# Kernel tuning notes

Measured on AMD Instinct MI355X. Metric: run time of the kernel, lower is better.

Reference implementation:

```python
import jax, jax.numpy as jnp
import numpy as np


def setup_inputs() -> dict:
    key = jax.random.key(0)
    k1, k2 = jax.random.split(key)
    z = jax.random.normal(k1, (16, 256, 32, 32), dtype=jnp.float32)
    emb = jax.random.normal(k2, (8192, 256), dtype=jnp.float32)
    return {"z": z, "emb": emb}


def reference(z, emb):
    B, C, H, W = z.shape
    # [B,C,H,W] -> [B*H*W, C], distances in fp32 for precision
    z_f = jnp.transpose(z, (0, 2, 3, 1)).reshape(-1, C).astype(jnp.float32)
    e = emb.astype(jnp.float32)
    # squared-distance expansion: ||z||^2 - 2 z.e + ||e||^2  -> [N, K]
    d = (
        jnp.sum(z_f * z_f, axis=1, keepdims=True)
        - 2.0 * (z_f @ e.T)
        + jnp.sum(e * e, axis=1)[None, :]
    )
    idx = jnp.argmin(d, axis=1)  # [N]
    out = emb[idx].astype(z.dtype)  # codebook gather
    return jnp.transpose(out.reshape(B, H, W, C), (0, 3, 1, 2))
```

## Files before the change

kernel.cpp:

```cpp
#include <hip/hip_runtime.h>
#include <stdint.h>

#define NB   16
#define CD   256
#define HW   1024
#define NQ   16384
#define KCN  8192

typedef unsigned long long u64;
typedef unsigned short     u16;
using f32x4  = __attribute__((ext_vector_type(4))) float;
using bf16x8 = __attribute__((ext_vector_type(8))) __bf16;

#define ZTB_OFF  0
#define EMBB_OFF 8388608
#define EH_OFF   12582912
#define CAND_OFF 12615680

static __device__ __forceinline__ void gl_lds16(const void* g, void* l) {
  __builtin_amdgcn_global_load_lds(
      (const __attribute__((address_space(1))) void*)g,
      (__attribute__((address_space(3))) void*)l, 16, 0, 0);
}

static __device__ __forceinline__ unsigned bf16r(float x) {
  unsigned u = __float_as_uint(x);
  return (u + 0x7fffu + ((u >> 16) & 1u)) >> 16;
}

static __device__ __forceinline__ u64 umin64(u64 a, u64 b) { return a < b ? a : b; }
static __device__ __forceinline__ u64 umax64(u64 a, u64 b) { return a < b ? b : a; }

__global__ __launch_bounds__(256) void k_prep(const float* __restrict__ z,
                                              const float* __restrict__ emb,
                                              u16* __restrict__ zTb,
                                              u16* __restrict__ embB,
                                              float* __restrict__ eH) {
  const int bx = (int)blockIdx.x;
  if (bx < 1024) {
    __shared__ float tile[64][65];
    const int b   = bx >> 6;
    const int hwT = (bx >> 2) & 15;
    const int cT  = bx & 3;
    const int tx  = threadIdx.x & 63;
    const int ty  = threadIdx.x >> 6;
    const float* src = z + (size_t)(b * CD + cT * 64) * HW + hwT * 64;
#pragma unroll
    for (int i = 0; i < 16; ++i) {
      const int c_l = ty + 4 * i;
      tile[c_l][tx] = src[(size_t)c_l * HW + tx];
    }
    __syncthreads();
    const size_t dbase = (size_t)(b * HW + hwT * 64) * CD + cT * 64;
#pragma unroll
    for (int i = 0; i < 16; ++i) {
      const int hw_l = ty + 4 * i;
      zTb[dbase + (size_t)hw_l * CD + tx] = (u16)bf16r(tile[tx][hw_l]);
    }
  } else {
    const int wave = (bx - 1024) * 4 + ((int)threadIdx.x >> 6);
    const int lane = threadIdx.x & 63;
#pragma unroll
    for (int it = 0; it < 8; ++it) {
      const int row = wave * 8 + it;
      const float4 v = *(const float4*)(emb + (size_t)row * CD + lane * 4);
      uint2 pk;
      pk.x = bf16r(v.x) | (bf16r(v.y) << 16);
      pk.y = bf16r(v.z) | (bf16r(v.w) << 16);
      *(uint2*)(embB + (size_t)row * CD + lane * 4) = pk;
      float s = v.x * v.x + v.y * v.y + v.z * v.z + v.w * v.w;
#pragma unroll
      for (int off = 32; off; off >>= 1) s += __shfl_xor(s, off, 64);
      if (lane == 0) eH[row] = 0.5f * s + 1024.0f;
    }
  }
}

#define NT  8
#define BKC 4

__global__ __launch_bounds__(256, 2) void k_argmin(const u16* __restrict__ zTb,
                                                   const u16* __restrict__ embB,
                                                   const float* __restrict__ eH,
                                                   u64* __restrict__ cand) {
  __shared__ __align__(16) u16 As[128 * 64];
  __shared__ __align__(16) u16 Bs[128 * 64];
  const int tid  = threadIdx.x;
  const int w    = tid >> 6;
  const int lane = tid & 63;
  const int l15  = lane & 15, quad = lane >> 4, l7 = lane & 7;
  const int q0    = (int)(blockIdx.x >> 3) * 128;
  const int split = (int)(blockIdx.x & 7);
  const int wq0 = (w & 1) * 64, wn0 = (w >> 1) * 64, wh = w >> 1;

  const int srow  = w * 32 + (lane >> 3);
  const int scol8 = (l7 ^ (lane >> 3)) * 8;
  const int ldsL  = w * 4096 + lane * 16;
  const int co0 = ((0 * 4 + quad) ^ l7) * 16;
  const int co1 = ((1 * 4 + quad) ^ l7) * 16;

  const float FMAX = __uint_as_float(0x7F7FFFFFu);
  float b1[16], b2[16];
#pragma unroll
  for (int s = 0; s < 16; ++s) { b1[s] = FMAX; b2[s] = FMAX; }

  for (int nt = 0; nt < NT; ++nt) {
    const int n0 = split * 1024 + nt * 128;
    float eh[4];
#pragma unroll
    for (int j = 0; j < 4; ++j) eh[j] = eH[n0 + wn0 + 16 * j + l15];

    f32x4 acc[4][4];
#pragma unroll
    for (int i = 0; i < 4; ++i)
#pragma unroll
      for (int j = 0; j < 4; ++j) acc[i][j] = f32x4{0.f, 0.f, 0.f, 0.f};

    for (int kc = 0; kc < BKC; ++kc) {
#pragma unroll
      for (int i = 0; i < 4; ++i) {
        const int row = srow + i * 8;
        gl_lds16(zTb  + (size_t)(q0 + row) * CD + kc * 64 + scol8,
                 (char*)As + ldsL + i * 1024);
        gl_lds16(embB + (size_t)(n0 + row) * CD + kc * 64 + scol8,
                 (char*)Bs + ldsL + i * 1024);
      }
      __syncthreads();
#pragma unroll
      for (int ks = 0; ks < 2; ++ks) {
        const int co = ks ? co1 : co0;
        bf16x8 af[4], bfr[4];
#pragma unroll
        for (int i = 0; i < 4; ++i)
          af[i] = *(const bf16x8*)((const char*)As + (wq0 + i * 16 + l15) * 128 + co);
#pragma unroll
        for (int j = 0; j < 4; ++j)
          bfr[j] = *(const bf16x8*)((const char*)Bs + (wn0 + j * 16 + l15) * 128 + co);
#pragma unroll
        for (int i = 0; i < 4; ++i)
#pragma unroll
          for (int j = 0; j < 4; ++j)
            acc[i][j] = __builtin_amdgcn_mfma_f32_16x16x32_bf16(af[i], bfr[j],
                                                                acc[i][j], 0, 0, 0);
      }
      __syncthreads();
    }
#pragma unroll
    for (int i = 0; i < 4; ++i) {
#pragma unroll
      for (int r = 0; r < 4; ++r) {
        const int s = i * 4 + r;
        float kq[4];
#pragma unroll
        for (int j = 0; j < 4; ++j) {
          const unsigned kb = (__float_as_uint(eh[j] - acc[i][j][r]) & ~31u)
                              | (unsigned)(nt * 4 + j);
          kq[j] = __uint_as_float(kb);
        }
        const float lo01 = fminf(kq[0], kq[1]), hi01 = fmaxf(kq[0], kq[1]);
        const float lo23 = fminf(kq[2], kq[3]), hi23 = fmaxf(kq[2], kq[3]);
        const float best = fminf(lo01, lo23);
        const float sec  = fminf(fmaxf(lo01, lo23), fminf(hi01, hi23));
        b2[s] = fminf(fmaxf(best, b1[s]), fminf(sec, b2[s]));
        b1[s] = fminf(best, b1[s]);
      }
    }
  }
#pragma unroll
  for (int s = 0; s < 16; ++s) {
    u64 x1 = ((u64)__float_as_uint(b1[s]) << 32) | (unsigned)l15;
    u64 x2 = ((u64)__float_as_uint(b2[s]) << 32) | (unsigned)l15;
#pragma unroll
    for (int off = 1; off < 16; off <<= 1) {
      const u64 o1 = __shfl_xor(x1, off, 64);
      const u64 o2 = __shfl_xor(x2, off, 64);
      const u64 lo = umin64(x1, o1);
      const u64 hi = umax64(x1, o1);
      x1 = lo;
      x2 = umin64(hi, umin64(x2, o2));
    }
    if (l15 == 0) {
      const int i = s >> 2, r = s & 3;
      const int q = q0 + wq0 + i * 16 + quad * 4 + r;
      const unsigned kb1 = (unsigned)(x1 >> 32), kb2 = (unsigned)(x2 >> 32);
      const int n1 = split * 1024 + (int)((kb1 >> 2) & 7) * 128 + wn0
                     + 16 * (int)(kb1 & 3) + (int)(x1 & 15);
      const int n2 = split * 1024 + (int)((kb2 >> 2) & 7) * 128 + wn0
                     + 16 * (int)(kb2 & 3) + (int)(x2 & 15);
      cand[(size_t)q * 32 + split * 4 + wh * 2 + 0] = ((u64)kb1 << 32) | (unsigned)n1;
      cand[(size_t)q * 32 + split * 4 + wh * 2 + 1] = ((u64)kb2 << 32) | (unsigned)n2;
    }
  }
}

__global__ __launch_bounds__(256) void k_pick_out(const float* __restrict__ z,
                                                  const float* __restrict__ emb,
                                                  const u64* __restrict__ cand,
                                                  float* __restrict__ out) {
  __shared__ float zs[16][257];
  __shared__ float tile[16][257];
  const int t    = (int)threadIdx.x;
  const int lane = t & 63;
  const int wv   = t >> 6;
  const int sub  = lane >> 4;
  const int l15  = lane & 15;
  const int q0b  = (int)blockIdx.x * 16;
  const int b    = q0b >> 10, hw0 = q0b & 1023;
  const int q    = q0b + wv * 4 + sub;
  const int hwl  = wv * 4 + sub;

  {
    const float* zp = z + ((size_t)(b * CD + t)) * HW + hw0;
    const float4 a0 = *(const float4*)(zp + 0);
    const float4 a1 = *(const float4*)(zp + 4);
    const float4 a2 = *(const float4*)(zp + 8);
    const float4 a3 = *(const float4*)(zp + 12);
    zs[0][t] = a0.x;  zs[1][t] = a0.y;  zs[2][t] = a0.z;  zs[3][t] = a0.w;
    zs[4][t] = a1.x;  zs[5][t] = a1.y;  zs[6][t] = a1.z;  zs[7][t] = a1.w;
    zs[8][t] = a2.x;  zs[9][t] = a2.y;  zs[10][t] = a2.z; zs[11][t] = a2.w;
    zs[12][t] = a3.x; zs[13][t] = a3.y; zs[14][t] = a3.z; zs[15][t] = a3.w;
  }
  __syncthreads();

  const u64* cp = cand + (size_t)q * 32 + l15 * 2;
  const u64 v0 = cp[0], v1 = cp[1];
  u64 s0 = umin64(v0, v1), s1 = umax64(v0, v1), s2 = ~0ull, s3 = ~0ull;
#pragma unroll
  for (int off = 1; off < 16; off <<= 1) {
    const u64 b0 = __shfl_xor(s0, off, 64);
    const u64 b1 = __shfl_xor(s1, off, 64);
    const u64 b2 = __shfl_xor(s2, off, 64);
    const u64 b3 = __shfl_xor(s3, off, 64);
    const u64 c0 = umin64(s0, b0);
    const u64 c1 = umin64(umin64(s1, b1), umax64(s0, b0));
    const u64 c2 = umin64(umin64(s2, b2),
                          umin64(umax64(s1, b0), umax64(s0, b1)));
    const u64 c3 = umin64(umin64(umin64(s3, b3), umax64(s2, b0)),
                          umin64(umax64(s0, b2), umax64(s1, b1)));
    s0 = c0; s1 = c1; s2 = c2; s3 = c3;
  }
  const u64 sel[4] = {s0, s1, s2, s3};

  float zq[16];
#pragma unroll
  for (int j = 0; j < 16; ++j) zq[j] = zs[hwl][j * 16 + l15];

  double bd = 1e300;
  int bi = 0x7fffffff;
  float keep[16];
#pragma unroll
  for (int j = 0; j < 16; ++j) keep[j] = 0.f;
#pragma unroll
  for (int c4 = 0; c4 < 4; ++c4) {
    const int idx = (int)(unsigned)(sel[c4] & 0xffffffffull);
    const float* er = emb + (size_t)idx * CD;
    float ev[16];
#pragma unroll
    for (int j = 0; j < 16; ++j) ev[j] = er[j * 16 + l15];
    double s = 0.0;
#pragma unroll
    for (int j = 0; j < 16; ++j) {
      const double d = (double)zq[j] - (double)ev[j];
      s += d * d;
    }
#pragma unroll
    for (int off = 1; off < 16; off <<= 1) s += __shfl_xor(s, off, 64);
    const bool better = (s < bd) || (s == bd && idx < bi);
    if (better) {
      bd = s; bi = idx;
#pragma unroll
      for (int j = 0; j < 16; ++j) keep[j] = ev[j];
    }
  }
#pragma unroll
  for (int j = 0; j < 16; ++j) tile[hwl][j * 16 + l15] = keep[j];
  __syncthreads();
  const int cluster = t >> 4;
  const int ll      = t & 15;
  float* obase = out + (size_t)b * CD * HW + hw0 + ll;
#pragma unroll
  for (int j = 0; j < 16; ++j) {
    const int c = 16 * j + cluster;
    obase[(size_t)c * HW] = tile[ll][c];
  }
}

extern "C" void kernel_launch(void* const* d_in, const int* in_sizes, int n_in,
                              void* d_out, int out_size, void* d_ws, size_t ws_size,
                              hipStream_t stream) {
  const float* z   = (const float*)d_in[0];
  const float* emb = (const float*)d_in[1];
  float* out = (float*)d_out;

  char* ws = (char*)d_ws;
  u16*   zTb  = (u16*)(ws + ZTB_OFF);
  u16*   embB = (u16*)(ws + EMBB_OFF);
  float* eH   = (float*)(ws + EH_OFF);
  u64*   cand = (u64*)(ws + CAND_OFF);

  k_prep<<<1280, 256, 0, stream>>>(z, emb, zTb, embB, eH);
  k_argmin<<<1024, 256, 0, stream>>>(zTb, embB, eH, cand);
  k_pick_out<<<1024, 256, 0, stream>>>(z, emb, cand, out);
}
```

Baseline: 181.8 us.

## Load query operand directly into registers with double-buffered prefetch, drop A LDS tile

The query (A) tile is no longer staged through shared memory. Each wave loads its MFMA A fragments straight from global memory into registers and prefetches the next k-chunk into a second register buffer while the current one is consumed. Only the codebook (B) tile still goes through LDS. This halves LDS traffic and footprint, but A is reloaded from global/L2 every n-tile (8 times) and register pressure rises, which could hurt the 2-blocks-per-CU occupancy target.

Measured after the change: 214.2 us. 1.18x slower.

```diff
diff --git a/kernel.cpp b/kernel.cpp
--- a/kernel.cpp
+++ b/kernel.cpp
@@ -77,13 +77,11 @@
 }
 
 #define NT  8
-#define BKC 4
 
 __global__ __launch_bounds__(256, 2) void k_argmin(const u16* __restrict__ zTb,
                                                    const u16* __restrict__ embB,
                                                    const float* __restrict__ eH,
                                                    u64* __restrict__ cand) {
-  __shared__ __align__(16) u16 As[128 * 64];
   __shared__ __align__(16) u16 Bs[128 * 64];
   const int tid  = threadIdx.x;
   const int w    = tid >> 6;
@@ -93,16 +91,58 @@
   const int split = (int)(blockIdx.x & 7);
   const int wq0 = (w & 1) * 64, wn0 = (w >> 1) * 64, wh = w >> 1;
 
-  const int srow  = w * 32 + (lane >> 3);
+  const int srowB = w * 32 + (lane >> 3);
   const int scol8 = (l7 ^ (lane >> 3)) * 8;
   const int ldsL  = w * 4096 + lane * 16;
   const int co0 = ((0 * 4 + quad) ^ l7) * 16;
   const int co1 = ((1 * 4 + quad) ^ l7) * 16;
 
+  const u16* abase = zTb + (size_t)(q0 + wq0 + l15) * CD + quad * 8;
+
   const float FMAX = __uint_as_float(0x7F7FFFFFu);
   float b1[16], b2[16];
 #pragma unroll
   for (int s = 0; s < 16; ++s) { b1[s] = FMAX; b2[s] = FMAX; }
+
+  f32x4 acc[4][4];
+
+  bf16x8 aA[8], aB[8];
+#pragma unroll
+  for (int i = 0; i < 4; ++i)
+#pragma unroll
+    for (int ks = 0; ks < 2; ++ks)
+      aA[i * 2 + ks] = *(const bf16x8*)(abase + (size_t)i * 16 * CD + ks * 32);
+
+#define KSTEP(CUR, NXT, KC, KCN)                                                   \
+  do {                                                                             \
+    _Pragma("unroll")                                                              \
+    for (int i = 0; i < 4; ++i)                                                    \
+      gl_lds16(embB + (size_t)(n0 + srowB + i * 8) * CD + (KC) * 64 + scol8,       \
+               (char*)Bs + ldsL + i * 1024);                                       \
+    _Pragma("unroll")                                                              \
+    for (int i = 0; i < 4; ++i)                                                    \
+      _Pragma("unroll")                                                            \
+      for (int ks = 0; ks < 2; ++ks)                                               \
+        NXT[i * 2 + ks] =                                                          \
+            *(const bf16x8*)(abase + (size_t)i * 16 * CD + (KCN) * 64 + ks * 32);  \
+    __syncthreads();                                                               \
+    _Pragma("unroll")                                                              \
+    for (int ks = 0; ks < 2; ++ks) {                                               \
+      const int co = ks ? co1 : co0;                                               \
+      bf16x8 bfr[4];                                                               \
+      _Pragma("unroll")                                                            \
+      for (int j = 0; j < 4; ++j)                                                  \
+        bfr[j] = *(const bf16x8*)((const char*)Bs + (wn0 + j * 16 + l15) * 128 + co); \
+      _Pragma("unroll")                                                            \
+      for (int i = 0; i < 4; ++i)                                                  \
+        _Pragma("unroll")                                                          \
+        for (int j = 0; j < 4; ++j)                                                \
+          acc[i][j] = __builtin_amdgcn_mfma_f32_16x16x32_bf16(CUR[i * 2 + ks],     \
+                                                              bfr[j], acc[i][j],   \
+                                                              0, 0, 0);            \
+    }                                                                              \
+    __syncthreads();                                                               \
+  } while (0)
 
   for (int nt = 0; nt < NT; ++nt) {
     const int n0 = split * 1024 + nt * 128;
@@ -110,41 +150,16 @@
 #pragma unroll
     for (int j = 0; j < 4; ++j) eh[j] = eH[n0 + wn0 + 16 * j + l15];
 
-    f32x4 acc[4][4];
 #pragma unroll
     for (int i = 0; i < 4; ++i)
 #pragma unroll
       for (int j = 0; j < 4; ++j) acc[i][j] = f32x4{0.f, 0.f, 0.f, 0.f};
 
-    for (int kc = 0; kc < BKC; ++kc) {
-#pragma unroll
-      for (int i = 0; i < 4; ++i) {
-        const int row = srow + i * 8;
-        gl_lds16(zTb  + (size_t)(q0 + row) * CD + kc * 64 + scol8,
-                 (char*)As + ldsL + i * 1024);
-        gl_lds16(embB + (size_t)(n0 + row) * CD + kc * 64 + scol8,
-                 (char*)Bs + ldsL + i * 1024);
-      }
-      __syncthreads();
-#pragma unroll
-      for (int ks = 0; ks < 2; ++ks) {
-        const int co = ks ? co1 : co0;
-        bf16x8 af[4], bfr[4];
-#pragma unroll
-        for (int i = 0; i < 4; ++i)
-          af[i] = *(const bf16x8*)((const char*)As + (wq0 + i * 16 + l15) * 128 + co);
-#pragma unroll
-        for (int j = 0; j < 4; ++j)
-          bfr[j] = *(const bf16x8*)((const char*)Bs + (wn0 + j * 16 + l15) * 128 + co);
-#pragma unroll
-        for (int i = 0; i < 4; ++i)
-#pragma unroll
-          for (int j = 0; j < 4; ++j)
-            acc[i][j] = __builtin_amdgcn_mfma_f32_16x16x32_bf16(af[i], bfr[j],
-                                                                acc[i][j], 0, 0, 0);
-      }
-      __syncthreads();
-    }
+    KSTEP(aA, aB, 0, 1);
+    KSTEP(aB, aA, 1, 2);
+    KSTEP(aA, aB, 2, 3);
+    KSTEP(aB, aA, 3, 0);
+
 #pragma unroll
     for (int i = 0; i < 4; ++i) {
 #pragma unroll
@@ -166,6 +181,8 @@
       }
     }
   }
+#undef KSTEP
+
 #pragma unroll
   for (int s = 0; s < 16; ++s) {
     u64 x1 = ((u64)__float_as_uint(b1[s]) << 32) | (unsigned)l15;
```

## Double-buffer LDS tiles to overlap global-to-LDS loads with MFMA compute

Applied to the files above, without the earlier changes.

Adds a second pair of shared-memory A/B tiles and prefetches the next K chunk (including the first chunk of the next N tile) into the idle buffer while MFMAs run on the current one. This removes the serialized load, sync, compute pattern and one barrier per K step. It doubles LDS use to 64KB per block, which may reduce occupancy under launch_bounds(256,2). The final iteration issues a redundant prefetch, and correctness depends on the direct-to-LDS loads having completed by the barrier.

Result: faster. 177.9 us (-2.2%).

```diff
diff --git a/kernel.cpp b/kernel.cpp
--- a/kernel.cpp
+++ b/kernel.cpp
@@ -77,14 +77,15 @@
 }
 
 #define NT  8
-#define BKC 4
 
 __global__ __launch_bounds__(256, 2) void k_argmin(const u16* __restrict__ zTb,
                                                    const u16* __restrict__ embB,
                                                    const float* __restrict__ eH,
                                                    u64* __restrict__ cand) {
-  __shared__ __align__(16) u16 As[128 * 64];
-  __shared__ __align__(16) u16 Bs[128 * 64];
+  __shared__ __align__(16) u16 As0[128 * 64];
+  __shared__ __align__(16) u16 Bs0[128 * 64];
+  __shared__ __align__(16) u16 As1[128 * 64];
+  __shared__ __align__(16) u16 Bs1[128 * 64];
   const int tid  = threadIdx.x;
   const int w    = tid >> 6;
   const int lane = tid & 63;
@@ -104,47 +105,68 @@
 #pragma unroll
   for (int s = 0; s < 16; ++s) { b1[s] = FMAX; b2[s] = FMAX; }
 
+  f32x4 acc[4][4];
+
+  {
+    const int n0i = split * 1024;
+#pragma unroll
+    for (int i = 0; i < 4; ++i) {
+      const int row = srow + i * 8;
+      gl_lds16(zTb  + (size_t)(q0 + row) * CD + 0 * 64 + scol8,
+               (char*)As0 + ldsL + i * 1024);
+      gl_lds16(embB + (size_t)(n0i + row) * CD + 0 * 64 + scol8,
+               (char*)Bs0 + ldsL + i * 1024);
+    }
+  }
+  __syncthreads();
+
+#define KSTEP(PA, PB, NA, NBuf, NKC, NN0)                                            \
+  do {                                                                               \
+    _Pragma("unroll")                                                                \
+    for (int i = 0; i < 4; ++i) {                                                    \
+      const int row = srow + i * 8;                                                  \
+      gl_lds16(zTb  + (size_t)(q0 + row) * CD + (NKC) * 64 + scol8,                  \
+               (char*)NA + ldsL + i * 1024);                                         \
+      gl_lds16(embB + (size_t)((NN0) + row) * CD + (NKC) * 64 + scol8,               \
+               (char*)NBuf + ldsL + i * 1024);                                       \
+    }                                                                                \
+    _Pragma("unroll")                                                                \
+    for (int ks = 0; ks < 2; ++ks) {                                                 \
+      const int co = ks ? co1 : co0;                                                 \
+      bf16x8 af[4], bfr[4];                                                          \
+      _Pragma("unroll")                                                              \
+      for (int i = 0; i < 4; ++i)                                                    \
+        af[i] = *(const bf16x8*)((const char*)PA + (wq0 + i * 16 + l15) * 128 + co); \
+      _Pragma("unroll")                                                              \
+      for (int j = 0; j < 4; ++j)                                                    \
+        bfr[j] = *(const bf16x8*)((const char*)PB + (wn0 + j * 16 + l15) * 128 + co);\
+      _Pragma("unroll")                                                              \
+      for (int i = 0; i < 4; ++i)                                                    \
+        _Pragma("unroll")                                                            \
+        for (int j = 0; j < 4; ++j)                                                  \
+          acc[i][j] = __builtin_amdgcn_mfma_f32_16x16x32_bf16(af[i], bfr[j],         \
+                                                              acc[i][j], 0, 0, 0);   \
+    }                                                                                \
+    __syncthreads();                                                                 \
+  } while (0)
+
   for (int nt = 0; nt < NT; ++nt) {
-    const int n0 = split * 1024 + nt * 128;
+    const int n0  = split * 1024 + nt * 128;
+    const int n0n = (nt == NT - 1) ? n0 : n0 + 128;
     float eh[4];
 #pragma unroll
     for (int j = 0; j < 4; ++j) eh[j] = eH[n0 + wn0 + 16 * j + l15];
 
-    f32x4 acc[4][4];
 #pragma unroll
     for (int i = 0; i < 4; ++i)
 #pragma unroll
       for (int j = 0; j < 4; ++j) acc[i][j] = f32x4{0.f, 0.f, 0.f, 0.f};
 
-    for (int kc = 0; kc < BKC; ++kc) {
-#pragma unroll
-      for (int i = 0; i < 4; ++i) {
-        const int row = srow + i * 8;
-        gl_lds16(zTb  + (size_t)(q0 + row) * CD + kc * 64 + scol8,
-                 (char*)As + ldsL + i * 1024);
-        gl_lds16(embB + (size_t)(n0 + row) * CD + kc * 64 + scol8,
-                 (char*)Bs + ldsL + i * 1024);
-      }
-      __syncthreads();
-#pragma unroll
-      for (int ks = 0; ks < 2; ++ks) {
-        const int co = ks ? co1 : co0;
-        bf16x8 af[4], bfr[4];
-#pragma unroll
-        for (int i = 0; i < 4; ++i)
-          af[i] = *(const bf16x8*)((const char*)As + (wq0 + i * 16 + l15) * 128 + co);
-#pragma unroll
-        for (int j = 0; j < 4; ++j)
-          bfr[j] = *(const bf16x8*)((const char*)Bs + (wn0 + j * 16 + l15) * 128 + co);
-#pragma unroll
-        for (int i = 0; i < 4; ++i)
-#pragma unroll
-          for (int j = 0; j < 4; ++j)
-            acc[i][j] = __builtin_amdgcn_mfma_f32_16x16x32_bf16(af[i], bfr[j],
-                                                                acc[i][j], 0, 0, 0);
-      }
-      __syncthreads();
-    }
+    KSTEP(As0, Bs0, As1, Bs1, 1, n0);
+    KSTEP(As1, Bs1, As0, Bs0, 2, n0);
+    KSTEP(As0, Bs0, As1, Bs1, 3, n0);
+    KSTEP(As1, Bs1, As0, Bs0, 0, n0n);
+
 #pragma unroll
     for (int i = 0; i < 4; ++i) {
 #pragma unroll
@@ -166,6 +188,8 @@
       }
     }
   }
+#undef KSTEP
+
 #pragma unroll
   for (int s = 0; s < 16; ++s) {
     u64 x1 = ((u64)__float_as_uint(b1[s]) << 32) | (unsigned)l15;
```
